# Kernel optimization log

Hardware: AMD Instinct MI355X
Metric: run time of the kernel (lower is better)

Reference implementation:

```python
import jax, jax.numpy as jnp
import numpy as np

EPS = 1e-5  # torch.nn.LayerNorm default

def layernorm(x, gamma, beta):
    mu = jnp.mean(x, axis=-1, keepdims=True)
    var = jnp.mean(jnp.square(x - mu), axis=-1, keepdims=True)
    return (x - mu) * jax.lax.rsqrt(var + EPS) * gamma + beta

def setup_inputs() -> dict:
    key = jax.random.key(0)
    ks = jax.random.split(key, 5)
    B, H = 8192, 1024
    stdv = 1.0 / np.sqrt(H)
    inp = jax.random.normal(ks[0], (B, 4 * H), dtype=jnp.float32)
    hx = jax.random.normal(ks[1], (B, H), dtype=jnp.float32)
    cx = jax.random.normal(ks[2], (B, H), dtype=jnp.float32)
    weight_hh = jax.random.uniform(ks[3], (4 * H, H), dtype=jnp.float32, minval=-stdv, maxval=stdv)
    gamma_h = jnp.ones((4 * H,), jnp.float32)
    beta_h = jnp.zeros((4 * H,), jnp.float32)
    gamma_c = jnp.ones((H,), jnp.float32)
    beta_c = jnp.zeros((H,), jnp.float32)
    return {"input": inp, "hx": hx, "cx": cx, "weight_hh": weight_hh,
            "gamma_h": gamma_h, "beta_h": beta_h, "gamma_c": gamma_c, "beta_c": beta_c}

def reference(input, hx, cx, weight_hh, gamma_h, beta_h, gamma_c, beta_c):
    # hgates = LN(hx @ W_hh^T); gates = igates + hgates
    hgates = layernorm(jnp.matmul(hx, weight_hh.T), gamma_h, beta_h)
    gates = input + hgates  # [B, 4H]
    i_g, f_g, c_g, o_g = jnp.split(gates, 4, axis=1)
    ingate = jax.nn.sigmoid(i_g)
    forgetgate = jax.nn.sigmoid(f_g)
    cellgate = jnp.tanh(c_g)
    outgate = jax.nn.sigmoid(o_g)
    cy = layernorm(forgetgate * cx + ingate * cellgate, gamma_c, beta_c)
    hy = outgate * jnp.tanh(cy)
    return (hy, cy)
```

## Files before the change

### kernel.cpp

```cpp
#include <hip/hip_runtime.h>
#include <hip/hip_bf16.h>

typedef __attribute__((ext_vector_type(8))) short short8;
typedef __attribute__((ext_vector_type(4))) float f32x4;

#define LN_EPS 1e-5f

__device__ __forceinline__ ushort f32_to_bf16(float f) {
  union { float f; unsigned u; } v; v.f = f;
  unsigned u = v.u;
  u += 0x7FFFu + ((u >> 16) & 1u);
  return (ushort)(u >> 16);
}
__device__ __forceinline__ float bf16_to_f32(ushort h) {
  union { unsigned u; float f; } v; v.u = ((unsigned)h) << 16; return v.f;
}
__device__ __forceinline__ float sigmoid_f(float x) {
  return 1.0f / (1.0f + __expf(-x));
}
__device__ __forceinline__ float tanh_f(float x) {
  return 2.0f / (1.0f + __expf(-2.0f * x)) - 1.0f;
}

__device__ __forceinline__ void gload16(const ushort* g, ushort* l) {
  __builtin_amdgcn_global_load_lds(
      (const __attribute__((address_space(1))) unsigned int*)g,
      (__attribute__((address_space(3))) unsigned int*)l, 16, 0, 0);
}

__global__ __launch_bounds__(256) void cast2_f32_bf16(
    const float* __restrict__ a, ushort* __restrict__ oa, int na4,
    const float* __restrict__ b, ushort* __restrict__ ob, int nb4) {
  int i = blockIdx.x * 256 + threadIdx.x;
  int stride = gridDim.x * 256;
  for (; i < na4 + nb4; i += stride) {
    const float* src = (i < na4) ? a : b;
    ushort* dst = (i < na4) ? oa : ob;
    int k = (i < na4) ? i : i - na4;
    float4 v = ((const float4*)src)[k];
    ushort4 o;
    o.x = f32_to_bf16(v.x); o.y = f32_to_bf16(v.y);
    o.z = f32_to_bf16(v.z); o.w = f32_to_bf16(v.w);
    ((ushort4*)dst)[k] = o;
  }
}

#define DS_A(QM)                                                            \
  _Pragma("unroll") for (int ks = 0; ks < 2; ks++)                          \
  _Pragma("unroll") for (int m = 0; m < 4; m++)                             \
    af[ks][m] = *(const short8*)&Acur[aoff[ks] + (QM) * 4096 + m * 1024];
#define DS_B(QN)                                                            \
  _Pragma("unroll") for (int ks = 0; ks < 2; ks++)                          \
  _Pragma("unroll") for (int n = 0; n < 2; n++)                             \
    bf_[ks][n] = *(const short8*)&Bcur[boff[ks] + (QN) * 2048 + n * 1024];
#define MFMAS(QM, QN)                                                       \
  _Pragma("unroll") for (int ks = 0; ks < 2; ks++)                          \
  _Pragma("unroll") for (int m = 0; m < 4; m++)                             \
  _Pragma("unroll") for (int n = 0; n < 2; n++)                             \
    acc[(QM) * 4 + m][(QN) * 2 + n] = __builtin_amdgcn_mfma_f32_16x16x32_bf16( \
        af[ks][m], bf_[ks][n], acc[(QM) * 4 + m][(QN) * 2 + n], 0, 0, 0);
#define PHASE_SYNC_PRE()                                                    \
  __builtin_amdgcn_s_barrier();                                             \
  asm volatile("s_waitcnt lgkmcnt(0)" ::: "memory");                        \
  __builtin_amdgcn_sched_barrier(0);                                        \
  __builtin_amdgcn_s_setprio(1);
#define PHASE_SYNC_POST()                                                   \
  __builtin_amdgcn_s_setprio(0);                                            \
  __builtin_amdgcn_s_barrier();

__global__ __launch_bounds__(512, 2) void gemm_bt(const ushort* __restrict__ A,
                                                  const ushort* __restrict__ B,
                                                  ushort* __restrict__ C,
                                                  int M, int N, int K) {
  __shared__ alignas(16) ushort lds[65536];
  const int tid = threadIdx.x;
  const int l = tid & 63;
  const int wv = tid >> 6;
  const int wm = wv >> 2, wn = wv & 3;

  const int nwg = gridDim.x;
  const int cpx = nwg >> 3;
  const int bid = blockIdx.x;
  const int swz = (bid & 7) * cpx + (bid >> 3);
  const int nbn = N >> 8;
  const int bm = swz / nbn;
  const int bn = swz % nbn;

  f32x4 acc[8][4];
#pragma unroll
  for (int i = 0; i < 8; i++)
#pragma unroll
    for (int j = 0; j < 4; j++) acc[i][j] = (f32x4){0.f, 0.f, 0.f, 0.f};

  const int lc = (tid & 7) ^ ((tid >> 3) & 7);
  const ushort* srcA0 = A + (size_t)(bm * 256 + (tid >> 3)) * K + lc * 8;
  const ushort* srcB0 = B + (size_t)(bn * 256 + (tid >> 3)) * K + lc * 8;
  ushort* dstA0 = lds + tid * 8;
  ushort* dstB0 = lds + 32768 + tid * 8;
#define STAGE(BUFSEL, KCOL)                                                 \
  _Pragma("unroll") for (int l2 = 0; l2 < 4; l2++) {                        \
    gload16(srcA0 + (size_t)l2 * 64 * K + (KCOL), dstA0 + (BUFSEL) * 16384 + l2 * 4096); \
    gload16(srcB0 + (size_t)l2 * 64 * K + (KCOL), dstB0 + (BUFSEL) * 16384 + l2 * 4096); \
  }

  const int lr = l & 15;
  const int lg = l >> 4;
  const int lx = l & 7;
  int aoff[2], boff[2];
#pragma unroll
  for (int ks = 0; ks < 2; ks++) {
    const int pc = ((ks << 2) | lg) ^ lx;
    aoff[ks] = (wm * 128 + lr) * 64 + pc * 8;
    boff[ks] = (wn * 64 + lr) * 64 + pc * 8;
  }

  STAGE(0, 0);
  asm volatile("s_waitcnt vmcnt(0)" ::: "memory");
  __builtin_amdgcn_s_barrier();

  const int NT = K >> 6;
  for (int t = 0; t < NT; ++t) {
    const ushort* Acur = lds + (t & 1) * 16384;
    const ushort* Bcur = lds + 32768 + (t & 1) * 16384;
    const int nbuf = (t & 1) ^ 1;
    short8 af[2][4], bf_[2][2];

    DS_A(0); DS_B(0);
    if (t < NT - 1) { STAGE(nbuf, (t + 1) * 64); }
    PHASE_SYNC_PRE();
    MFMAS(0, 0);
    PHASE_SYNC_POST();

    DS_B(1);
    PHASE_SYNC_PRE();
    MFMAS(0, 1);
    PHASE_SYNC_POST();

    DS_A(1);
    PHASE_SYNC_PRE();
    MFMAS(1, 1);
    PHASE_SYNC_POST();

    DS_B(0);
    PHASE_SYNC_PRE();
    MFMAS(1, 0);
    __builtin_amdgcn_s_setprio(0);
    asm volatile("s_waitcnt vmcnt(0)" ::: "memory");
    __builtin_amdgcn_s_barrier();
  }

#pragma unroll
  for (int mi = 0; mi < 8; mi++) {
    const int rowb = bm * 256 + wm * 128 + mi * 16 + lg * 4;
#pragma unroll
    for (int ni = 0; ni < 4; ni++) {
      const int col = bn * 256 + wn * 64 + ni * 16 + lr;
#pragma unroll
      for (int r = 0; r < 4; r++)
        C[(size_t)(rowb + r) * N + col] = f32_to_bf16(acc[mi][ni][r]);
    }
  }
}

__global__ __launch_bounds__(256) void lstm_ln_kernel(
    const ushort* __restrict__ gates_pre,
    const float* __restrict__ input,
    const float* __restrict__ cx,
    const float* __restrict__ gamma_h, const float* __restrict__ beta_h,
    const float* __restrict__ gamma_c, const float* __restrict__ beta_c,
    float* __restrict__ hy, float* __restrict__ cy, int H) {
  const int FH = 4 * H;
  const int row = blockIdx.x;
  const int t = threadIdx.x;
  const int lane = t & 63, wv = t >> 6;
  const int j0 = t * 4;
  __shared__ float redA[8], redB[8];

  const ushort* gp = gates_pre + (size_t)row * FH;

  float xg[4][4];
#pragma unroll
  for (int g = 0; g < 4; g++) {
    ushort4 u = *(const ushort4*)(gp + g * H + j0);
    xg[g][0] = bf16_to_f32(u.x); xg[g][1] = bf16_to_f32(u.y);
    xg[g][2] = bf16_to_f32(u.z); xg[g][3] = bf16_to_f32(u.w);
  }

  float s1 = 0.f, s2 = 0.f;
#pragma unroll
  for (int g = 0; g < 4; g++)
#pragma unroll
    for (int q = 0; q < 4; q++) { s1 += xg[g][q]; s2 += xg[g][q] * xg[g][q]; }
  {
    float a = s1, b = s2;
#pragma unroll
    for (int off = 32; off > 0; off >>= 1) {
      a += __shfl_down(a, off, 64);
      b += __shfl_down(b, off, 64);
    }
    if (lane == 0) { redA[wv] = a; redA[4 + wv] = b; }
  }
  __syncthreads();
  const float inv_fh = 1.0f / (float)FH;
  const float mu  = (redA[0] + redA[1] + redA[2] + redA[3]) * inv_fh;
  const float m2  = (redA[4] + redA[5] + redA[6] + redA[7]) * inv_fh;
  const float rstd = rsqrtf(m2 - mu * mu + LN_EPS);

  const float* ip = input + (size_t)row * FH;
  float a_g[4][4];
#pragma unroll
  for (int g = 0; g < 4; g++) {
    float4 iv = *(const float4*)(ip + g * H + j0);
    float4 gv = *(const float4*)(gamma_h + g * H + j0);
    float4 bv = *(const float4*)(beta_h + g * H + j0);
    a_g[g][0] = (xg[g][0] - mu) * rstd * gv.x + bv.x + iv.x;
    a_g[g][1] = (xg[g][1] - mu) * rstd * gv.y + bv.y + iv.y;
    a_g[g][2] = (xg[g][2] - mu) * rstd * gv.z + bv.z + iv.z;
    a_g[g][3] = (xg[g][3] - mu) * rstd * gv.w + bv.w + iv.w;
  }

  float4 cxv = *(const float4*)(cx + (size_t)row * H + j0);
  const float* cxa = (const float*)&cxv;
  float cell[4], og[4];
  float s3 = 0.f, s4 = 0.f;
#pragma unroll
  for (int q = 0; q < 4; q++) {
    float in_s = sigmoid_f(a_g[0][q]);
    float fg_s = sigmoid_f(a_g[1][q]);
    float cg_t = tanh_f(a_g[2][q]);
    og[q] = sigmoid_f(a_g[3][q]);
    float cl = fg_s * cxa[q] + in_s * cg_t;
    cell[q] = cl;
    s3 += cl; s4 += cl * cl;
  }
  {
    float a = s3, b = s4;
#pragma unroll
    for (int off = 32; off > 0; off >>= 1) {
      a += __shfl_down(a, off, 64);
      b += __shfl_down(b, off, 64);
    }
    if (lane == 0) { redB[wv] = a; redB[4 + wv] = b; }
  }
  __syncthreads();
  const float inv_h = 1.0f / (float)H;
  const float mu2   = (redB[0] + redB[1] + redB[2] + redB[3]) * inv_h;
  const float m22   = (redB[4] + redB[5] + redB[6] + redB[7]) * inv_h;
  const float rstd2 = rsqrtf(m22 - mu2 * mu2 + LN_EPS);

  float4 gc = *(const float4*)(gamma_c + j0);
  float4 bc = *(const float4*)(beta_c + j0);
  const float* gca = (const float*)&gc;
  const float* bca = (const float*)&bc;
  float4 cyo, hyo;
  float* cyp = (float*)&cyo; float* hyp = (float*)&hyo;
#pragma unroll
  for (int q = 0; q < 4; q++) {
    float cyv = (cell[q] - mu2) * rstd2 * gca[q] + bca[q];
    cyp[q] = cyv;
    hyp[q] = og[q] * tanh_f(cyv);
  }
  *(float4*)(cy + (size_t)row * H + j0) = cyo;
  *(float4*)(hy + (size_t)row * H + j0) = hyo;
}

extern "C" void kernel_launch(void* const* d_in, const int* in_sizes, int n_in,
                              void* d_out, int out_size, void* d_ws, size_t ws_size,
                              hipStream_t stream) {
  (void)n_in; (void)out_size; (void)ws_size;
  const float* input   = (const float*)d_in[0];
  const float* hx      = (const float*)d_in[1];
  const float* cx      = (const float*)d_in[2];
  const float* w       = (const float*)d_in[3];
  const float* gamma_h = (const float*)d_in[4];
  const float* beta_h  = (const float*)d_in[5];
  const float* gamma_c = (const float*)d_in[6];
  const float* beta_c  = (const float*)d_in[7];

  const int H  = in_sizes[6];
  const int B  = in_sizes[1] / H;
  const int FH = 4 * H;
  const int K  = H;

  ushort* hx_bf = (ushort*)d_ws;
  ushort* w_bf  = hx_bf + (size_t)B * K;
  ushort* gates = w_bf + (size_t)FH * K;

  float* hy = (float*)d_out;
  float* cy = hy + (size_t)B * H;

  cast2_f32_bf16<<<2048, 256, 0, stream>>>(hx, hx_bf, (B * K) / 4,
                                           w, w_bf, (FH * K) / 4);

  const int nblocks = (B / 256) * (FH / 256);
  gemm_bt<<<nblocks, 512, 0, stream>>>(hx_bf, w_bf, gates, B, FH, K);

  lstm_ln_kernel<<<B, 256, 0, stream>>>(gates, input, cx, gamma_h, beta_h,
                                        gamma_c, beta_c, hy, cy, H);
}
```

Baseline: 350.8 us.

## Interleave quarter-tile global prefetch with MFMA phases using fine-grained vmcnt waits

The GEMM's next-tile prefetch is split into four half-A/half-B loads, each issued in one of the four MFMA phases. Each phase waits with a partial vmcnt instead of a single full drain at the end of the iteration. The LDS layout and accumulator indexing are reorganised so each staged piece maps to a quadrant read in a later phase, and the last iteration is peeled. The goal is smoother overlap of global loads with compute, at the cost of more complex synchronisation that depends on exact vmcnt bookkeeping.

```diff
diff --git a/kernel.cpp b/kernel.cpp
--- a/kernel.cpp
+++ b/kernel.cpp
@@ -48,23 +48,34 @@
 #define DS_A(QM)                                                            \
   _Pragma("unroll") for (int ks = 0; ks < 2; ks++)                          \
   _Pragma("unroll") for (int m = 0; m < 4; m++)                             \
-    af[ks][m] = *(const short8*)&Acur[aoff[ks] + (QM) * 4096 + m * 1024];
+    af[ks][m] = *(const short8*)&lds[bufo + (QM) * 8192 + aoffs[ks] + m * 1024];
 #define DS_B(QN)                                                            \
   _Pragma("unroll") for (int ks = 0; ks < 2; ks++)                          \
   _Pragma("unroll") for (int n = 0; n < 2; n++)                             \
-    bf_[ks][n] = *(const short8*)&Bcur[boff[ks] + (QN) * 2048 + n * 1024];
+    bf_[ks][n] = *(const short8*)&lds[32768 + bufo + (QN) * 8192 + boffs[ks] + n * 1024];
 #define MFMAS(QM, QN)                                                       \
   _Pragma("unroll") for (int ks = 0; ks < 2; ks++)                          \
   _Pragma("unroll") for (int m = 0; m < 4; m++)                             \
   _Pragma("unroll") for (int n = 0; n < 2; n++)                             \
-    acc[(QM) * 4 + m][(QN) * 2 + n] = __builtin_amdgcn_mfma_f32_16x16x32_bf16( \
-        af[ks][m], bf_[ks][n], acc[(QM) * 4 + m][(QN) * 2 + n], 0, 0, 0);
-#define PHASE_SYNC_PRE()                                                    \
+    acc[QM][m][QN][n] = __builtin_amdgcn_mfma_f32_16x16x32_bf16(            \
+        af[ks][m], bf_[ks][n], acc[QM][m][QN][n], 0, 0, 0);
+#define STAGE_A(bsel, h, kc)                                                \
+  { gload16(A + (size_t)(bm * 256 + (h) * 64 + arow0) * K + (kc) + lc8,     \
+            lds + (bsel) * 16384 + (h) * 8192 + tid * 8);                   \
+    gload16(A + (size_t)(bm * 256 + (h) * 64 + 128 + arow0) * K + (kc) + lc8, \
+            lds + (bsel) * 16384 + (h) * 8192 + 4096 + tid * 8); }
+#define STAGE_B(bsel, h, kc)                                                \
+  { gload16(B + (size_t)(bn * 256 + (h) * 32 + brow0) * K + (kc) + lc8,     \
+            lds + 32768 + (bsel) * 16384 + (h) * 8192 + tid * 8);           \
+    gload16(B + (size_t)(bn * 256 + (h) * 32 + brow0 + 128) * K + (kc) + lc8, \
+            lds + 32768 + (bsel) * 16384 + (h) * 8192 + 4096 + tid * 8); }
+#define SYNC_PRE(VNSTR)                                                     \
+  asm volatile("s_waitcnt vmcnt(" VNSTR ")" ::: "memory");                  \
   __builtin_amdgcn_s_barrier();                                             \
   asm volatile("s_waitcnt lgkmcnt(0)" ::: "memory");                        \
   __builtin_amdgcn_sched_barrier(0);                                        \
   __builtin_amdgcn_s_setprio(1);
-#define PHASE_SYNC_POST()                                                   \
+#define SYNC_POST()                                                         \
   __builtin_amdgcn_s_setprio(0);                                            \
   __builtin_amdgcn_s_barrier();
 
@@ -86,80 +97,113 @@
   const int bm = swz / nbn;
   const int bn = swz % nbn;
 
-  f32x4 acc[8][4];
-#pragma unroll
-  for (int i = 0; i < 8; i++)
-#pragma unroll
-    for (int j = 0; j < 4; j++) acc[i][j] = (f32x4){0.f, 0.f, 0.f, 0.f};
-
-  const int lc = (tid & 7) ^ ((tid >> 3) & 7);
-  const ushort* srcA0 = A + (size_t)(bm * 256 + (tid >> 3)) * K + lc * 8;
-  const ushort* srcB0 = B + (size_t)(bn * 256 + (tid >> 3)) * K + lc * 8;
-  ushort* dstA0 = lds + tid * 8;
-  ushort* dstB0 = lds + 32768 + tid * 8;
-#define STAGE(BUFSEL, KCOL)                                                 \
-  _Pragma("unroll") for (int l2 = 0; l2 < 4; l2++) {                        \
-    gload16(srcA0 + (size_t)l2 * 64 * K + (KCOL), dstA0 + (BUFSEL) * 16384 + l2 * 4096); \
-    gload16(srcB0 + (size_t)l2 * 64 * K + (KCOL), dstB0 + (BUFSEL) * 16384 + l2 * 4096); \
-  }
+  f32x4 acc[2][4][2][2];
+#pragma unroll
+  for (int qm = 0; qm < 2; qm++)
+#pragma unroll
+    for (int m = 0; m < 4; m++)
+#pragma unroll
+      for (int qn = 0; qn < 2; qn++)
+#pragma unroll
+        for (int n = 0; n < 2; n++) acc[qm][m][qn][n] = (f32x4){0.f, 0.f, 0.f, 0.f};
+
+  const int arow0 = tid >> 3;
+  const int q8 = tid >> 3;
+  const int brow0 = (q8 & 31) + ((q8 >> 5) << 6);
+  const int lc8 = ((tid & 7) ^ ((tid >> 3) & 7)) * 8;
 
   const int lr = l & 15;
-  const int lg = l >> 4;
+  const int lg = (l >> 4) & 3;
   const int lx = l & 7;
-  int aoff[2], boff[2];
+  int aoffs[2], boffs[2];
 #pragma unroll
   for (int ks = 0; ks < 2; ks++) {
     const int pc = ((ks << 2) | lg) ^ lx;
-    aoff[ks] = (wm * 128 + lr) * 64 + pc * 8;
-    boff[ks] = (wn * 64 + lr) * 64 + pc * 8;
-  }
-
-  STAGE(0, 0);
+    aoffs[ks] = (wm * 64 + lr) * 64 + pc * 8;
+    boffs[ks] = (wn * 32 + lr) * 64 + pc * 8;
+  }
+
+  STAGE_A(0, 0, 0);
+  STAGE_B(0, 0, 0);
+  STAGE_B(0, 1, 0);
+  STAGE_A(0, 1, 0);
   asm volatile("s_waitcnt vmcnt(0)" ::: "memory");
   __builtin_amdgcn_s_barrier();
 
   const int NT = K >> 6;
-  for (int t = 0; t < NT; ++t) {
-    const ushort* Acur = lds + (t & 1) * 16384;
-    const ushort* Bcur = lds + 32768 + (t & 1) * 16384;
-    const int nbuf = (t & 1) ^ 1;
+  for (int t = 0; t < NT - 1; ++t) {
+    const int bufo = (t & 1) * 16384;
+    const int nb = (t + 1) & 1;
+    const int kc = (t + 1) << 6;
     short8 af[2][4], bf_[2][2];
 
     DS_A(0); DS_B(0);
-    if (t < NT - 1) { STAGE(nbuf, (t + 1) * 64); }
-    PHASE_SYNC_PRE();
+    STAGE_A(nb, 0, kc);
+    SYNC_PRE("4");
     MFMAS(0, 0);
-    PHASE_SYNC_POST();
+    SYNC_POST();
 
     DS_B(1);
-    PHASE_SYNC_PRE();
+    STAGE_B(nb, 0, kc);
+    SYNC_PRE("4");
     MFMAS(0, 1);
-    PHASE_SYNC_POST();
+    SYNC_POST();
 
     DS_A(1);
-    PHASE_SYNC_PRE();
+    STAGE_B(nb, 1, kc);
+    SYNC_PRE("6");
     MFMAS(1, 1);
-    PHASE_SYNC_POST();
+    SYNC_POST();
 
     DS_B(0);
-    PHASE_SYNC_PRE();
+    STAGE_A(nb, 1, kc);
+    SYNC_PRE("4");
     MFMAS(1, 0);
-    __builtin_amdgcn_s_setprio(0);
-    asm volatile("s_waitcnt vmcnt(0)" ::: "memory");
+    SYNC_POST();
+  }
+
+  {
+    const int t = NT - 1;
+    const int bufo = (t & 1) * 16384;
+    short8 af[2][4], bf_[2][2];
+
+    DS_A(0); DS_B(0);
+    SYNC_PRE("2");
+    MFMAS(0, 0);
+    SYNC_POST();
+
+    DS_B(1);
+    SYNC_PRE("0");
+    MFMAS(0, 1);
+    SYNC_POST();
+
+    DS_A(1);
+    SYNC_PRE("0");
+    MFMAS(1, 1);
+    SYNC_POST();
+
+    DS_B(0);
     __builtin_amdgcn_s_barrier();
-  }
-
-#pragma unroll
-  for (int mi = 0; mi < 8; mi++) {
-    const int rowb = bm * 256 + wm * 128 + mi * 16 + lg * 4;
-#pragma unroll
-    for (int ni = 0; ni < 4; ni++) {
-      const int col = bn * 256 + wn * 64 + ni * 16 + lr;
-#pragma unroll
-      for (int r = 0; r < 4; r++)
-        C[(size_t)(rowb + r) * N + col] = f32_to_bf16(acc[mi][ni][r]);
+    asm volatile("s_waitcnt lgkmcnt(0)" ::: "memory");
+    __builtin_amdgcn_sched_barrier(0);
+    MFMAS(1, 0);
+  }
+
+#pragma unroll
+  for (int qm = 0; qm < 2; qm++)
+#pragma unroll
+    for (int m = 0; m < 4; m++) {
+      const int rowb = bm * 256 + wm * 128 + qm * 64 + m * 16 + lg * 4;
+#pragma unroll
+      for (int qn = 0; qn < 2; qn++)
+#pragma unroll
+        for (int n = 0; n < 2; n++) {
+          const int col = bn * 256 + wn * 64 + qn * 32 + n * 16 + lr;
+#pragma unroll
+          for (int r = 0; r < 4; r++)
+            C[(size_t)(rowb + r) * N + col] = f32_to_bf16(acc[qm][m][qn][n][r]);
+        }
     }
-  }
 }
 
 __global__ __launch_bounds__(256) void lstm_ln_kernel(
```

New measurement: 344.4 us. Within noise of the previous version (-1.8%).
